# Performance work log

Hardware: AMD Instinct MI355X
Metric: run time of the kernel (lower is better)

Reference implementation:

```python
import jax, jax.numpy as jnp
import numpy as np

B, N, D = 8, 256, 256
LN_EPS = 1e-5


def setup_inputs() -> dict:
    key = jax.random.key(0)
    ks = jax.random.split(key, 8)
    s1 = 1.0 / np.sqrt(2 * D)  # torch Linear init scale ~ U(-1/sqrt(fan_in), ...); use normal*scale
    s2 = 1.0 / np.sqrt(D)
    return {
        "patch_features": jax.random.normal(ks[0], (B, N, D), dtype=jnp.float32),
        # relation_transform: Linear(2D, D) -> ReLU -> Linear(D, 1)
        "W1": jax.random.normal(ks[1], (2 * D, D), dtype=jnp.float32) * s1,
        "b1": jax.random.normal(ks[2], (D,), dtype=jnp.float32) * s1,
        "W2": jax.random.normal(ks[3], (D, 1), dtype=jnp.float32) * s2,
        "b2": jax.random.normal(ks[4], (1,), dtype=jnp.float32) * s2,
        # context_projection: Linear(D, D) + LayerNorm(D)
        "Wp": jax.random.normal(ks[5], (D, D), dtype=jnp.float32) * s2,
        "bp": jax.random.normal(ks[6], (D,), dtype=jnp.float32) * s2,
        "ln_gamma": jnp.ones((D,), dtype=jnp.float32),
        "ln_beta": jnp.zeros((D,), dtype=jnp.float32),
    }


def reference(patch_features, W1, b1, W2, b2, Wp, bp, ln_gamma, ln_beta):
    x = patch_features  # [B, N, D]
    d = x.shape[-1]
    # cat([x_i, x_j]) @ W1 == x_i @ W1[:D] + x_j @ W1[D:]
    hi = jnp.einsum("bnd,de->bne", x, W1[:d])   # [B, N, D]
    hj = jnp.einsum("bmd,de->bme", x, W1[d:])   # [B, N, D]
    h = jax.nn.relu(hi[:, :, None, :] + hj[:, None, :, :] + b1)  # [B, N, N, D]
    scores = jnp.einsum("bnmd,do->bnm", h, W2) + b2[0]            # [B, N, N]
    # diagonal entries stay exactly 0 (original never fills i == j)
    eye = jnp.eye(scores.shape[1], dtype=bool)
    scores = jnp.where(eye[None, :, :], 0.0, scores)
    weights = jax.nn.softmax(scores, axis=2)                      # [B, N, N]
    ctx = jnp.einsum("bnm,bmd->bnd", weights, x)                  # [B, N, D]
    proj = jnp.einsum("bnd,de->bne", ctx, Wp) + bp
    mu = jnp.mean(proj, axis=-1, keepdims=True)
    var = jnp.mean(jnp.square(proj - mu), axis=-1, keepdims=True)
    ln = (proj - mu) * jax.lax.rsqrt(var + LN_EPS) * ln_gamma + ln_beta
    return x + ln
```

## Files before the change

### kernel.cpp

```cpp
#include <hip/hip_runtime.h>

#define LN_EPS 1e-5f

__device__ __forceinline__ float wred_max(float v) {
#pragma unroll
    for (int off = 32; off; off >>= 1) v = fmaxf(v, __shfl_xor(v, off, 64));
    return v;
}
__device__ __forceinline__ float wred_sum(float v) {
#pragma unroll
    for (int off = 32; off; off >>= 1) v += __shfl_xor(v, off, 64);
    return v;
}


#define GL(Q, KB) { const float* _p = Wb + (size_t)((KB) * 8) * 256;            \
    _Pragma("unroll") for (int _j = 0; _j < 8; _j++)                            \
        Q[_j] = *(const float2*)(_p + (size_t)_j * 256); }

#define GC(Q, KB) { const int _k = (KB) * 8;                                    \
    _Pragma("unroll") for (int _r = 0; _r < 4; _r++) {                          \
        float4 _xa = *(const float4*)&xs[_r][_k];                               \
        float4 _xb = *(const float4*)&xs[_r][_k + 4];                           \
        acc[_r][0] = fmaf(_xa.x, Q[0].x, acc[_r][0]);                           \
        acc[_r][1] = fmaf(_xa.x, Q[0].y, acc[_r][1]);                           \
        acc[_r][0] = fmaf(_xa.y, Q[1].x, acc[_r][0]);                           \
        acc[_r][1] = fmaf(_xa.y, Q[1].y, acc[_r][1]);                           \
        acc[_r][0] = fmaf(_xa.z, Q[2].x, acc[_r][0]);                           \
        acc[_r][1] = fmaf(_xa.z, Q[2].y, acc[_r][1]);                           \
        acc[_r][0] = fmaf(_xa.w, Q[3].x, acc[_r][0]);                           \
        acc[_r][1] = fmaf(_xa.w, Q[3].y, acc[_r][1]);                           \
        acc[_r][0] = fmaf(_xb.x, Q[4].x, acc[_r][0]);                           \
        acc[_r][1] = fmaf(_xb.x, Q[4].y, acc[_r][1]);                           \
        acc[_r][0] = fmaf(_xb.y, Q[5].x, acc[_r][0]);                           \
        acc[_r][1] = fmaf(_xb.y, Q[5].y, acc[_r][1]);                           \
        acc[_r][0] = fmaf(_xb.z, Q[6].x, acc[_r][0]);                           \
        acc[_r][1] = fmaf(_xb.z, Q[6].y, acc[_r][1]);                           \
        acc[_r][0] = fmaf(_xb.w, Q[7].x, acc[_r][0]);                           \
        acc[_r][1] = fmaf(_xb.w, Q[7].y, acc[_r][1]); } }

__global__ __launch_bounds__(256) void k_gemm_hij(
    const float* __restrict__ x,
    const float* __restrict__ W1,
    const float* __restrict__ b1,
    float* __restrict__ hi_ws,
    float* __restrict__ hjT)
{
    __shared__ __align__(16) float xs[4][256];
    const int t = threadIdx.x;
    const int lane = t & 63, w = t >> 6;
    const int b = blockIdx.x & 7;
    const int i = blockIdx.x >> 3;
    const int row0 = b * 256 + i * 4;

    ((float4*)xs)[t] = ((const float4*)(x + (size_t)row0 * 256))[t];
    __syncthreads();

    const int half = w >> 1;
    const int e0 = ((w & 1) << 7) + 2 * lane;
    const float* Wb = W1 + (size_t)half * 65536 + e0;

    float acc[4][2];
#pragma unroll
    for (int r = 0; r < 4; r++) { acc[r][0] = 0.f; acc[r][1] = 0.f; }

    float2 qa[8], qb[8];
    GL(qa, 0);
    for (int kb = 0; kb + 2 < 32; kb += 2) {
        GL(qb, kb + 1);
        GC(qa, kb);
        GL(qa, kb + 2);
        GC(qb, kb + 1);
    }
    GL(qb, 31);
    GC(qa, 30);
    GC(qb, 31);

    if (half == 0) {
        float2 bb = *(const float2*)(b1 + e0);
#pragma unroll
        for (int r = 0; r < 4; r++)
            *(float2*)&hi_ws[(size_t)(row0 + r) * 256 + e0] =
                make_float2(acc[r][0] + bb.x, acc[r][1] + bb.y);
    } else {
        const int m0 = i * 4;
        *(float4*)&hjT[(size_t)b * 65536 + (size_t)e0 * 256 + m0] =
            make_float4(acc[0][0], acc[1][0], acc[2][0], acc[3][0]);
        *(float4*)&hjT[(size_t)b * 65536 + (size_t)(e0 + 1) * 256 + m0] =
            make_float4(acc[0][1], acc[1][1], acc[2][1], acc[3][1]);
    }
}


#define P1L(H, G) { const float* _p = hjp + (size_t)((G) * 4) * 256;            \
    _Pragma("unroll") for (int _j = 0; _j < 4; _j++)                            \
        H[_j] = *(const float4*)(_p + (size_t)_j * 256); }

#define P1C(H, G) { const int _db = w * 64 + (G) * 4;                           \
    float4 _wq = *(const float4*)&w2_s[_db];                                    \
    _Pragma("unroll") for (int _n = 0; _n < 4; _n++) {                          \
        float4 _h4 = *(const float4*)&hi_s[_n][_db];                            \
        sp[_n][0] = fmaf(fmaxf(_h4.x + H[0].x, 0.f), _wq.x, sp[_n][0]);         \
        sp[_n][0] = fmaf(fmaxf(_h4.y + H[1].x, 0.f), _wq.y, sp[_n][0]);         \
        sp[_n][0] = fmaf(fmaxf(_h4.z + H[2].x, 0.f), _wq.z, sp[_n][0]);         \
        sp[_n][0] = fmaf(fmaxf(_h4.w + H[3].x, 0.f), _wq.w, sp[_n][0]);         \
        sp[_n][1] = fmaf(fmaxf(_h4.x + H[0].y, 0.f), _wq.x, sp[_n][1]);         \
        sp[_n][1] = fmaf(fmaxf(_h4.y + H[1].y, 0.f), _wq.y, sp[_n][1]);         \
        sp[_n][1] = fmaf(fmaxf(_h4.z + H[2].y, 0.f), _wq.z, sp[_n][1]);         \
        sp[_n][1] = fmaf(fmaxf(_h4.w + H[3].y, 0.f), _wq.w, sp[_n][1]);         \
        sp[_n][2] = fmaf(fmaxf(_h4.x + H[0].z, 0.f), _wq.x, sp[_n][2]);         \
        sp[_n][2] = fmaf(fmaxf(_h4.y + H[1].z, 0.f), _wq.y, sp[_n][2]);         \
        sp[_n][2] = fmaf(fmaxf(_h4.z + H[2].z, 0.f), _wq.z, sp[_n][2]);         \
        sp[_n][2] = fmaf(fmaxf(_h4.w + H[3].z, 0.f), _wq.w, sp[_n][2]);         \
        sp[_n][3] = fmaf(fmaxf(_h4.x + H[0].w, 0.f), _wq.x, sp[_n][3]);         \
        sp[_n][3] = fmaf(fmaxf(_h4.y + H[1].w, 0.f), _wq.y, sp[_n][3]);         \
        sp[_n][3] = fmaf(fmaxf(_h4.z + H[2].w, 0.f), _wq.z, sp[_n][3]);         \
        sp[_n][3] = fmaf(fmaxf(_h4.w + H[3].w, 0.f), _wq.w, sp[_n][3]); } }

#define DLOAD(X, PTR, G) { const float* _p = (PTR) + (size_t)((G) * 8) * 256;   \
    _Pragma("unroll") for (int _j = 0; _j < 8; _j++)                            \
        X[_j] = *(const float4*)(_p + (size_t)_j * 256); }

#define DCOMP(ACCV, WS, X, G) { const int _rb = w * 64 + (G) * 8;               \
    _Pragma("unroll") for (int _n = 0; _n < 4; _n++) {                          \
        float4 _wa = *(const float4*)&WS[_n][_rb];                              \
        float4 _wb = *(const float4*)&WS[_n][_rb + 4];                          \
        ACCV[_n][0] = fmaf(_wa.x, X[0].x, ACCV[_n][0]);                         \
        ACCV[_n][0] = fmaf(_wa.y, X[1].x, ACCV[_n][0]);                         \
        ACCV[_n][0] = fmaf(_wa.z, X[2].x, ACCV[_n][0]);                         \
        ACCV[_n][0] = fmaf(_wa.w, X[3].x, ACCV[_n][0]);                         \
        ACCV[_n][0] = fmaf(_wb.x, X[4].x, ACCV[_n][0]);                         \
        ACCV[_n][0] = fmaf(_wb.y, X[5].x, ACCV[_n][0]);                         \
        ACCV[_n][0] = fmaf(_wb.z, X[6].x, ACCV[_n][0]);                         \
        ACCV[_n][0] = fmaf(_wb.w, X[7].x, ACCV[_n][0]);                         \
        ACCV[_n][1] = fmaf(_wa.x, X[0].y, ACCV[_n][1]);                         \
        ACCV[_n][1] = fmaf(_wa.y, X[1].y, ACCV[_n][1]);                         \
        ACCV[_n][1] = fmaf(_wa.z, X[2].y, ACCV[_n][1]);                         \
        ACCV[_n][1] = fmaf(_wa.w, X[3].y, ACCV[_n][1]);                         \
        ACCV[_n][1] = fmaf(_wb.x, X[4].y, ACCV[_n][1]);                         \
        ACCV[_n][1] = fmaf(_wb.y, X[5].y, ACCV[_n][1]);                         \
        ACCV[_n][1] = fmaf(_wb.z, X[6].y, ACCV[_n][1]);                         \
        ACCV[_n][1] = fmaf(_wb.w, X[7].y, ACCV[_n][1]);                         \
        ACCV[_n][2] = fmaf(_wa.x, X[0].z, ACCV[_n][2]);                         \
        ACCV[_n][2] = fmaf(_wa.y, X[1].z, ACCV[_n][2]);                         \
        ACCV[_n][2] = fmaf(_wa.z, X[2].z, ACCV[_n][2]);                         \
        ACCV[_n][2] = fmaf(_wa.w, X[3].z, ACCV[_n][2]);                         \
        ACCV[_n][2] = fmaf(_wb.x, X[4].z, ACCV[_n][2]);                         \
        ACCV[_n][2] = fmaf(_wb.y, X[5].z, ACCV[_n][2]);                         \
        ACCV[_n][2] = fmaf(_wb.z, X[6].z, ACCV[_n][2]);                         \
        ACCV[_n][2] = fmaf(_wb.w, X[7].z, ACCV[_n][2]);                         \
        ACCV[_n][3] = fmaf(_wa.x, X[0].w, ACCV[_n][3]);                         \
        ACCV[_n][3] = fmaf(_wa.y, X[1].w, ACCV[_n][3]);                         \
        ACCV[_n][3] = fmaf(_wa.z, X[2].w, ACCV[_n][3]);                         \
        ACCV[_n][3] = fmaf(_wa.w, X[3].w, ACCV[_n][3]);                         \
        ACCV[_n][3] = fmaf(_wb.x, X[4].w, ACCV[_n][3]);                         \
        ACCV[_n][3] = fmaf(_wb.y, X[5].w, ACCV[_n][3]);                         \
        ACCV[_n][3] = fmaf(_wb.z, X[6].w, ACCV[_n][3]);                         \
        ACCV[_n][3] = fmaf(_wb.w, X[7].w, ACCV[_n][3]); } }

__global__ __launch_bounds__(256) void k_fused(
    const float* __restrict__ x,
    const float* __restrict__ hi_ws,
    const float* __restrict__ hjT,
    const float* __restrict__ W2, const float* __restrict__ b2,
    const float* __restrict__ Wp, const float* __restrict__ bp,
    const float* __restrict__ gma, const float* __restrict__ bta,
    float* __restrict__ out)
{
    const int t = threadIdx.x;
    const int lane = t & 63, w = t >> 6;
    const int b = blockIdx.x & 7;
    const int n0 = (blockIdx.x >> 3) * 4;
    const int bn0 = b * 256 + n0;

    __shared__ __align__(16) float hi_s[4][256];
    __shared__ __align__(16) float w2_s[256];
    __shared__ __align__(16) float wt_s[4][256];
    __shared__ __align__(16) float ctx_s[4][256];
    __shared__ __align__(16) float sred[4][4][256];
    __shared__ float part[8][4];

#pragma unroll
    for (int i = 0; i < 4; i++) hi_s[i][t] = hi_ws[(size_t)(bn0 + i) * 256 + t];
    w2_s[t] = W2[t];
    __syncthreads();

    {
        const float* hjp = hjT + (size_t)b * 65536 + (size_t)(w * 64) * 256 + 4 * lane;
        float sp[4][4];
#pragma unroll
        for (int n = 0; n < 4; n++)
#pragma unroll
            for (int j = 0; j < 4; j++) sp[n][j] = 0.f;

        float4 ha[4], hb[4];
        P1L(ha, 0);
        for (int g = 0; g + 2 < 16; g += 2) {
            P1L(hb, g + 1);
            P1C(ha, g);
            P1L(ha, g + 2);
            P1C(hb, g + 1);
        }
        P1L(hb, 15);
        P1C(ha, 14);
        P1C(hb, 15);

#pragma unroll
        for (int n = 0; n < 4; n++)
            *(float4*)&sred[w][n][4 * lane] =
                make_float4(sp[n][0], sp[n][1], sp[n][2], sp[n][3]);
    }
    __syncthreads();

    float b2v = b2[0];
    float s[4];
#pragma unroll
    for (int i = 0; i < 4; i++) {
        s[i] = ((sred[0][i][t] + sred[1][i][t]) +
                (sred[2][i][t] + sred[3][i][t])) + b2v;
        if (t == n0 + i) s[i] = 0.f;
    }
#pragma unroll
    for (int i = 0; i < 4; i++) {
        float m = wred_max(s[i]);
        if (lane == 0) part[i][w] = m;
    }
    __syncthreads();
    float ev[4];
#pragma unroll
    for (int i = 0; i < 4; i++) {
        float mx = fmaxf(fmaxf(part[i][0], part[i][1]),
                         fmaxf(part[i][2], part[i][3]));
        ev[i] = __expf(s[i] - mx);
        float sm = wred_sum(ev[i]);
        if (lane == 0) part[4 + i][w] = sm;
    }
    __syncthreads();
#pragma unroll
    for (int i = 0; i < 4; i++) {
        float tot = (part[4 + i][0] + part[4 + i][1]) +
                    (part[4 + i][2] + part[4 + i][3]);
        wt_s[i][t] = ev[i] / tot;
    }
    __syncthreads();

    {
        const float* xpp = x + (size_t)b * 65536 + (size_t)(w * 64) * 256 + 4 * lane;
        float cp[4][4];
#pragma unroll
        for (int n = 0; n < 4; n++)
#pragma unroll
            for (int j = 0; j < 4; j++) cp[n][j] = 0.f;

        float4 xa[8], xb[8];
        DLOAD(xa, xpp, 0);
        for (int g = 0; g + 2 < 8; g += 2) {
            DLOAD(xb, xpp, g + 1);
            DCOMP(cp, wt_s, xa, g);
            DLOAD(xa, xpp, g + 2);
            DCOMP(cp, wt_s, xb, g + 1);
        }
        DLOAD(xb, xpp, 7);
        DCOMP(cp, wt_s, xa, 6);
        DCOMP(cp, wt_s, xb, 7);

#pragma unroll
        for (int n = 0; n < 4; n++)
            *(float4*)&sred[w][n][4 * lane] =
                make_float4(cp[n][0], cp[n][1], cp[n][2], cp[n][3]);
    }
    __syncthreads();
#pragma unroll
    for (int i = 0; i < 4; i++)
        ctx_s[i][t] = (sred[0][i][t] + sred[1][i][t]) +
                      (sred[2][i][t] + sred[3][i][t]);
    __syncthreads();

    {
        const float* wpp = Wp + (size_t)(w * 64) * 256 + 4 * lane;
        float pq[4][4];
#pragma unroll
        for (int n = 0; n < 4; n++)
#pragma unroll
            for (int j = 0; j < 4; j++) pq[n][j] = 0.f;

        float4 qa4[8], qb4[8];
        DLOAD(qa4, wpp, 0);
        for (int g = 0; g + 2 < 8; g += 2) {
            DLOAD(qb4, wpp, g + 1);
            DCOMP(pq, ctx_s, qa4, g);
            DLOAD(qa4, wpp, g + 2);
            DCOMP(pq, ctx_s, qb4, g + 1);
        }
        DLOAD(qb4, wpp, 7);
        DCOMP(pq, ctx_s, qa4, 6);
        DCOMP(pq, ctx_s, qb4, 7);

#pragma unroll
        for (int n = 0; n < 4; n++)
            *(float4*)&sred[w][n][4 * lane] =
                make_float4(pq[n][0], pq[n][1], pq[n][2], pq[n][3]);
    }
    __syncthreads();

    float bpv = bp[t];
    float p[4];
#pragma unroll
    for (int i = 0; i < 4; i++)
        p[i] = ((sred[0][i][t] + sred[1][i][t]) +
                (sred[2][i][t] + sred[3][i][t])) + bpv;

#pragma unroll
    for (int i = 0; i < 4; i++) {
        float su = wred_sum(p[i]);
        float sq = wred_sum(p[i] * p[i]);
        if (lane == 0) { part[i][w] = su; part[4 + i][w] = sq; }
    }
    __syncthreads();
    float gv = gma[t], bv = bta[t];
#pragma unroll
    for (int i = 0; i < 4; i++) {
        float su = (part[i][0] + part[i][1]) + (part[i][2] + part[i][3]);
        float sq = (part[4 + i][0] + part[4 + i][1]) +
                   (part[4 + i][2] + part[4 + i][3]);
        float mu = su * (1.f / 256.f);
        float var = sq * (1.f / 256.f) - mu * mu;
        float ln = (p[i] - mu) * rsqrtf(var + LN_EPS) * gv + bv;
        out[(size_t)(bn0 + i) * 256 + t] = x[(size_t)(bn0 + i) * 256 + t] + ln;
    }
}

extern "C" void kernel_launch(void* const* d_in, const int* in_sizes, int n_in,
                              void* d_out, int out_size, void* d_ws, size_t ws_size,
                              hipStream_t stream) {
    const float* x   = (const float*)d_in[0];
    const float* W1  = (const float*)d_in[1];
    const float* b1  = (const float*)d_in[2];
    const float* W2  = (const float*)d_in[3];
    const float* b2  = (const float*)d_in[4];
    const float* Wp  = (const float*)d_in[5];
    const float* bp  = (const float*)d_in[6];
    const float* gma = (const float*)d_in[7];
    const float* bta = (const float*)d_in[8];
    float* out = (float*)d_out;

    float* hi_ws = (float*)d_ws;
    float* hjT   = hi_ws + (size_t)2048 * 256;

    k_gemm_hij<<<512, 256, 0, stream>>>(x, W1, b1, hi_ws, hjT);
    k_fused<<<512, 256, 0, stream>>>(x, hi_ws, hjT, W2, b2, Wp, bp,
                                     gma, bta, out);
}
```

Baseline: 107.5 us.

## Retile hij GEMM and widen fused kernel to 8 rows per 512-thread block

The first GEMM kernel is re-tiled so each wave computes 8 rows by 64 output columns. X rows are read directly from global memory (uniform per wave) instead of through shared memory, and W1 is loaded as scalar columns. The fused scoring/softmax/projection kernel now handles 8 query rows per block with 512 threads, so each thread reuses its loaded hjT, x and Wp values across twice as many rows, halving redundant global reads. The cost is more shared memory, extra barriers for the two-pass reductions, higher register pressure, and half as many blocks.

```diff
diff --git a/kernel.cpp b/kernel.cpp
--- a/kernel.cpp
+++ b/kernel.cpp
@@ -14,30 +14,13 @@
 }
 
 
-#define GL(Q, KB) { const float* _p = Wb + (size_t)((KB) * 8) * 256;            \
-    _Pragma("unroll") for (int _j = 0; _j < 8; _j++)                            \
-        Q[_j] = *(const float2*)(_p + (size_t)_j * 256); }
-
-#define GC(Q, KB) { const int _k = (KB) * 8;                                    \
-    _Pragma("unroll") for (int _r = 0; _r < 4; _r++) {                          \
-        float4 _xa = *(const float4*)&xs[_r][_k];                               \
-        float4 _xb = *(const float4*)&xs[_r][_k + 4];                           \
-        acc[_r][0] = fmaf(_xa.x, Q[0].x, acc[_r][0]);                           \
-        acc[_r][1] = fmaf(_xa.x, Q[0].y, acc[_r][1]);                           \
-        acc[_r][0] = fmaf(_xa.y, Q[1].x, acc[_r][0]);                           \
-        acc[_r][1] = fmaf(_xa.y, Q[1].y, acc[_r][1]);                           \
-        acc[_r][0] = fmaf(_xa.z, Q[2].x, acc[_r][0]);                           \
-        acc[_r][1] = fmaf(_xa.z, Q[2].y, acc[_r][1]);                           \
-        acc[_r][0] = fmaf(_xa.w, Q[3].x, acc[_r][0]);                           \
-        acc[_r][1] = fmaf(_xa.w, Q[3].y, acc[_r][1]);                           \
-        acc[_r][0] = fmaf(_xb.x, Q[4].x, acc[_r][0]);                           \
-        acc[_r][1] = fmaf(_xb.x, Q[4].y, acc[_r][1]);                           \
-        acc[_r][0] = fmaf(_xb.y, Q[5].x, acc[_r][0]);                           \
-        acc[_r][1] = fmaf(_xb.y, Q[5].y, acc[_r][1]);                           \
-        acc[_r][0] = fmaf(_xb.z, Q[6].x, acc[_r][0]);                           \
-        acc[_r][1] = fmaf(_xb.z, Q[6].y, acc[_r][1]);                           \
-        acc[_r][0] = fmaf(_xb.w, Q[7].x, acc[_r][0]);                           \
-        acc[_r][1] = fmaf(_xb.w, Q[7].y, acc[_r][1]); } }
+#define WL(Q, KB) { _Pragma("unroll") for (int _j = 0; _j < 8; _j++)            \
+        Q[_j] = Wc[(size_t)((KB) * 8 + _j) * 256]; }
+
+#define XC(Q, KB) { _Pragma("unroll") for (int _j = 0; _j < 8; _j++) {          \
+        const float _wj = Q[_j];                                                \
+        _Pragma("unroll") for (int _r = 0; _r < 8; _r++)                        \
+            acc[_r] = fmaf(xw[_r * 256 + (KB) * 8 + _j], _wj, acc[_r]); } }
 
 __global__ __launch_bounds__(256) void k_gemm_hij(
     const float* __restrict__ x,
@@ -46,48 +29,45 @@
     float* __restrict__ hi_ws,
     float* __restrict__ hjT)
 {
-    __shared__ __align__(16) float xs[4][256];
     const int t = threadIdx.x;
-    const int lane = t & 63, w = t >> 6;
-    const int b = blockIdx.x & 7;
-    const int i = blockIdx.x >> 3;
-    const int row0 = b * 256 + i * 4;
-
-    ((float4*)xs)[t] = ((const float4*)(x + (size_t)row0 * 256))[t];
-    __syncthreads();
-
-    const int half = w >> 1;
-    const int e0 = ((w & 1) << 7) + 2 * lane;
-    const float* Wb = W1 + (size_t)half * 65536 + e0;
-
-    float acc[4][2];
-#pragma unroll
-    for (int r = 0; r < 4; r++) { acc[r][0] = 0.f; acc[r][1] = 0.f; }
-
-    float2 qa[8], qb[8];
-    GL(qa, 0);
+    const int lane = t & 63;
+    const int w = __builtin_amdgcn_readfirstlane(t >> 6);
+    const int b  = blockIdx.x & 7;
+    const int rg = (blockIdx.x >> 3) & 7;
+    const int cg = blockIdx.x >> 6;
+
+    const int m0 = rg * 32 + w * 8;
+    const int row0 = b * 256 + m0;
+    const int e = cg * 64 + lane;
+
+    const float* xw = x + (size_t)row0 * 256;
+    const float* Wc = W1 + e + (e >= 256 ? 65280 : 0);
+
+    float acc[8];
+#pragma unroll
+    for (int r = 0; r < 8; r++) acc[r] = 0.f;
+
+    float qa[8], qb[8];
+    WL(qa, 0);
     for (int kb = 0; kb + 2 < 32; kb += 2) {
-        GL(qb, kb + 1);
-        GC(qa, kb);
-        GL(qa, kb + 2);
-        GC(qb, kb + 1);
-    }
-    GL(qb, 31);
-    GC(qa, 30);
-    GC(qb, 31);
-
-    if (half == 0) {
-        float2 bb = *(const float2*)(b1 + e0);
-#pragma unroll
-        for (int r = 0; r < 4; r++)
-            *(float2*)&hi_ws[(size_t)(row0 + r) * 256 + e0] =
-                make_float2(acc[r][0] + bb.x, acc[r][1] + bb.y);
+        WL(qb, kb + 1);
+        XC(qa, kb);
+        WL(qa, kb + 2);
+        XC(qb, kb + 1);
+    }
+    WL(qb, 31);
+    XC(qa, 30);
+    XC(qb, 31);
+
+    if (e < 256) {
+        const float bb = b1[e];
+#pragma unroll
+        for (int r = 0; r < 8; r++)
+            hi_ws[(size_t)(row0 + r) * 256 + e] = acc[r] + bb;
     } else {
-        const int m0 = i * 4;
-        *(float4*)&hjT[(size_t)b * 65536 + (size_t)e0 * 256 + m0] =
-            make_float4(acc[0][0], acc[1][0], acc[2][0], acc[3][0]);
-        *(float4*)&hjT[(size_t)b * 65536 + (size_t)(e0 + 1) * 256 + m0] =
-            make_float4(acc[0][1], acc[1][1], acc[2][1], acc[3][1]);
+        float* dst = hjT + (size_t)b * 65536 + (size_t)(e - 256) * 256 + m0;
+        *(float4*)dst       = make_float4(acc[0], acc[1], acc[2], acc[3]);
+        *(float4*)(dst + 4) = make_float4(acc[4], acc[5], acc[6], acc[7]);
     }
 }
 
@@ -96,9 +76,9 @@
     _Pragma("unroll") for (int _j = 0; _j < 4; _j++)                            \
         H[_j] = *(const float4*)(_p + (size_t)_j * 256); }
 
-#define P1C(H, G) { const int _db = w * 64 + (G) * 4;                           \
+#define P1C(H, G) { const int _db = w * 32 + (G) * 4;                           \
     float4 _wq = *(const float4*)&w2_s[_db];                                    \
-    _Pragma("unroll") for (int _n = 0; _n < 4; _n++) {                          \
+    _Pragma("unroll") for (int _n = 0; _n < 8; _n++) {                          \
         float4 _h4 = *(const float4*)&hi_s[_n][_db];                            \
         sp[_n][0] = fmaf(fmaxf(_h4.x + H[0].x, 0.f), _wq.x, sp[_n][0]);         \
         sp[_n][0] = fmaf(fmaxf(_h4.y + H[1].x, 0.f), _wq.y, sp[_n][0]);         \
@@ -121,8 +101,8 @@
     _Pragma("unroll") for (int _j = 0; _j < 8; _j++)                            \
         X[_j] = *(const float4*)(_p + (size_t)_j * 256); }
 
-#define DCOMP(ACCV, WS, X, G) { const int _rb = w * 64 + (G) * 8;               \
-    _Pragma("unroll") for (int _n = 0; _n < 4; _n++) {                          \
+#define DCOMP(ACCV, WS, X, G) { const int _rb = w * 32 + (G) * 8;               \
+    _Pragma("unroll") for (int _n = 0; _n < 8; _n++) {                          \
         float4 _wa = *(const float4*)&WS[_n][_rb];                              \
         float4 _wb = *(const float4*)&WS[_n][_rb + 4];                          \
         ACCV[_n][0] = fmaf(_wa.x, X[0].x, ACCV[_n][0]);                         \
@@ -158,7 +138,7 @@
         ACCV[_n][3] = fmaf(_wb.z, X[6].w, ACCV[_n][3]);                         \
         ACCV[_n][3] = fmaf(_wb.w, X[7].w, ACCV[_n][3]); } }
 
-__global__ __launch_bounds__(256) void k_fused(
+__global__ __launch_bounds__(512) void k_fused(
     const float* __restrict__ x,
     const float* __restrict__ hi_ws,
     const float* __restrict__ hjT,
@@ -170,163 +150,209 @@
     const int t = threadIdx.x;
     const int lane = t & 63, w = t >> 6;
     const int b = blockIdx.x & 7;
-    const int n0 = (blockIdx.x >> 3) * 4;
+    const int n0 = (blockIdx.x >> 3) * 8;
     const int bn0 = b * 256 + n0;
 
-    __shared__ __align__(16) float hi_s[4][256];
+    __shared__ __align__(16) float hi_s[8][256];
     __shared__ __align__(16) float w2_s[256];
-    __shared__ __align__(16) float wt_s[4][256];
-    __shared__ __align__(16) float ctx_s[4][256];
-    __shared__ __align__(16) float sred[4][4][256];
-    __shared__ float part[8][4];
-
-#pragma unroll
-    for (int i = 0; i < 4; i++) hi_s[i][t] = hi_ws[(size_t)(bn0 + i) * 256 + t];
-    w2_s[t] = W2[t];
+    __shared__ __align__(16) float wt_s[8][256];
+    __shared__ __align__(16) float ctx_s[8][256];
+    __shared__ __align__(16) float sred[8][4][256];
+    __shared__ float part_a[8][4], part_b[8][4];
+
+    ((float4*)hi_s)[t] = ((const float4*)(hi_ws + (size_t)bn0 * 256))[t];
+    if (t < 64) ((float4*)w2_s)[t] = ((const float4*)W2)[t];
     __syncthreads();
 
-    {
-        const float* hjp = hjT + (size_t)b * 65536 + (size_t)(w * 64) * 256 + 4 * lane;
-        float sp[4][4];
-#pragma unroll
-        for (int n = 0; n < 4; n++)
+    const int m = t & 255;
+    const int h = t >> 8;
+    const int wg = w & 3;
+
+    float sA[2], sB[2];
+    {
+        const float* hjp = hjT + (size_t)b * 65536 + (size_t)(w * 32) * 256 + 4 * lane;
+        float sp[8][4];
+#pragma unroll
+        for (int n = 0; n < 8; n++)
 #pragma unroll
             for (int j = 0; j < 4; j++) sp[n][j] = 0.f;
 
         float4 ha[4], hb[4];
         P1L(ha, 0);
-        for (int g = 0; g + 2 < 16; g += 2) {
-            P1L(hb, g + 1);
-            P1C(ha, g);
-            P1L(ha, g + 2);
-            P1C(hb, g + 1);
-        }
-        P1L(hb, 15);
-        P1C(ha, 14);
-        P1C(hb, 15);
-
+        P1L(hb, 1); P1C(ha, 0);
+        P1L(ha, 2); P1C(hb, 1);
+        P1L(hb, 3); P1C(ha, 2);
+        P1L(ha, 4); P1C(hb, 3);
+        P1L(hb, 5); P1C(ha, 4);
+        P1L(ha, 6); P1C(hb, 5);
+        P1L(hb, 7); P1C(ha, 6);
+        P1C(hb, 7);
+
+        const float b2v = b2[0];
 #pragma unroll
         for (int n = 0; n < 4; n++)
             *(float4*)&sred[w][n][4 * lane] =
                 make_float4(sp[n][0], sp[n][1], sp[n][2], sp[n][3]);
+        __syncthreads();
+#pragma unroll
+        for (int c = 0; c < 2; c++) {
+            const int n = 2 * h + c;
+            float v = ((sred[0][n][m] + sred[1][n][m]) + (sred[2][n][m] + sred[3][n][m])) +
+                      ((sred[4][n][m] + sred[5][n][m]) + (sred[6][n][m] + sred[7][n][m]));
+            v += b2v;
+            if (m == n0 + n) v = 0.f;
+            sA[c] = v;
+        }
+        __syncthreads();
+#pragma unroll
+        for (int n = 0; n < 4; n++)
+            *(float4*)&sred[w][n][4 * lane] =
+                make_float4(sp[4 + n][0], sp[4 + n][1], sp[4 + n][2], sp[4 + n][3]);
+        __syncthreads();
+#pragma unroll
+        for (int c = 0; c < 2; c++) {
+            const int nn = 2 * h + c;
+            float v = ((sred[0][nn][m] + sred[1][nn][m]) + (sred[2][nn][m] + sred[3][nn][m])) +
+                      ((sred[4][nn][m] + sred[5][nn][m]) + (sred[6][nn][m] + sred[7][nn][m]));
+            v += b2v;
+            if (m == n0 + 4 + nn) v = 0.f;
+            sB[c] = v;
+        }
+    }
+
+    {
+        const int ns[4] = {2 * h, 2 * h + 1, 4 + 2 * h, 4 + 2 * h + 1};
+        float s4[4] = {sA[0], sA[1], sB[0], sB[1]};
+        float ev4[4];
+#pragma unroll
+        for (int c = 0; c < 4; c++) {
+            const float mxw = wred_max(s4[c]);
+            if (lane == 0) part_a[ns[c]][wg] = mxw;
+        }
+        __syncthreads();
+#pragma unroll
+        for (int c = 0; c < 4; c++) {
+            const int n = ns[c];
+            const float mx = fmaxf(fmaxf(part_a[n][0], part_a[n][1]),
+                                   fmaxf(part_a[n][2], part_a[n][3]));
+            ev4[c] = __expf(s4[c] - mx);
+            const float sm = wred_sum(ev4[c]);
+            if (lane == 0) part_b[n][wg] = sm;
+        }
+        __syncthreads();
+#pragma unroll
+        for (int c = 0; c < 4; c++) {
+            const int n = ns[c];
+            const float tot = (part_b[n][0] + part_b[n][1]) + (part_b[n][2] + part_b[n][3]);
+            wt_s[n][m] = ev4[c] / tot;
+        }
     }
     __syncthreads();
 
-    float b2v = b2[0];
-    float s[4];
-#pragma unroll
-    for (int i = 0; i < 4; i++) {
-        s[i] = ((sred[0][i][t] + sred[1][i][t]) +
-                (sred[2][i][t] + sred[3][i][t])) + b2v;
-        if (t == n0 + i) s[i] = 0.f;
-    }
-#pragma unroll
-    for (int i = 0; i < 4; i++) {
-        float m = wred_max(s[i]);
-        if (lane == 0) part[i][w] = m;
-    }
-    __syncthreads();
-    float ev[4];
-#pragma unroll
-    for (int i = 0; i < 4; i++) {
-        float mx = fmaxf(fmaxf(part[i][0], part[i][1]),
-                         fmaxf(part[i][2], part[i][3]));
-        ev[i] = __expf(s[i] - mx);
-        float sm = wred_sum(ev[i]);
-        if (lane == 0) part[4 + i][w] = sm;
-    }
-    __syncthreads();
-#pragma unroll
-    for (int i = 0; i < 4; i++) {
-        float tot = (part[4 + i][0] + part[4 + i][1]) +
-                    (part[4 + i][2] + part[4 + i][3]);
-        wt_s[i][t] = ev[i] / tot;
-    }
-    __syncthreads();
-
-    {
-        const float* xpp = x + (size_t)b * 65536 + (size_t)(w * 64) * 256 + 4 * lane;
-        float cp[4][4];
-#pragma unroll
-        for (int n = 0; n < 4; n++)
+    {
+        const float* xpp = x + (size_t)b * 65536 + (size_t)(w * 32) * 256 + 4 * lane;
+        float cp[8][4];
+#pragma unroll
+        for (int n = 0; n < 8; n++)
 #pragma unroll
             for (int j = 0; j < 4; j++) cp[n][j] = 0.f;
 
         float4 xa[8], xb[8];
         DLOAD(xa, xpp, 0);
-        for (int g = 0; g + 2 < 8; g += 2) {
-            DLOAD(xb, xpp, g + 1);
-            DCOMP(cp, wt_s, xa, g);
-            DLOAD(xa, xpp, g + 2);
-            DCOMP(cp, wt_s, xb, g + 1);
-        }
-        DLOAD(xb, xpp, 7);
-        DCOMP(cp, wt_s, xa, 6);
-        DCOMP(cp, wt_s, xb, 7);
+        DLOAD(xb, xpp, 1); DCOMP(cp, wt_s, xa, 0);
+        DLOAD(xa, xpp, 2); DCOMP(cp, wt_s, xb, 1);
+        DLOAD(xb, xpp, 3); DCOMP(cp, wt_s, xa, 2);
+        DCOMP(cp, wt_s, xb, 3);
 
 #pragma unroll
         for (int n = 0; n < 4; n++)
             *(float4*)&sred[w][n][4 * lane] =
                 make_float4(cp[n][0], cp[n][1], cp[n][2], cp[n][3]);
+        __syncthreads();
+#pragma unroll
+        for (int c = 0; c < 2; c++) {
+            const int n = 2 * h + c;
+            ctx_s[n][m] = ((sred[0][n][m] + sred[1][n][m]) + (sred[2][n][m] + sred[3][n][m])) +
+                          ((sred[4][n][m] + sred[5][n][m]) + (sred[6][n][m] + sred[7][n][m]));
+        }
+        __syncthreads();
+#pragma unroll
+        for (int n = 0; n < 4; n++)
+            *(float4*)&sred[w][n][4 * lane] =
+                make_float4(cp[4 + n][0], cp[4 + n][1], cp[4 + n][2], cp[4 + n][3]);
+        __syncthreads();
+#pragma unroll
+        for (int c = 0; c < 2; c++) {
+            const int nn = 2 * h + c;
+            ctx_s[4 + nn][m] = ((sred[0][nn][m] + sred[1][nn][m]) + (sred[2][nn][m] + sred[3][nn][m])) +
+                               ((sred[4][nn][m] + sred[5][nn][m]) + (sred[6][nn][m] + sred[7][nn][m]));
+        }
     }
     __syncthreads();
-#pragma unroll
-    for (int i = 0; i < 4; i++)
-        ctx_s[i][t] = (sred[0][i][t] + sred[1][i][t]) +
-                      (sred[2][i][t] + sred[3][i][t]);
-    __syncthreads();
-
-    {
-        const float* wpp = Wp + (size_t)(w * 64) * 256 + 4 * lane;
-        float pq[4][4];
-#pragma unroll
-        for (int n = 0; n < 4; n++)
+
+    float p4[4];
+    {
+        const float* wpp = Wp + (size_t)(w * 32) * 256 + 4 * lane;
+        float pq[8][4];
+#pragma unroll
+        for (int n = 0; n < 8; n++)
 #pragma unroll
             for (int j = 0; j < 4; j++) pq[n][j] = 0.f;
 
         float4 qa4[8], qb4[8];
         DLOAD(qa4, wpp, 0);
-        for (int g = 0; g + 2 < 8; g += 2) {
-            DLOAD(qb4, wpp, g + 1);
-            DCOMP(pq, ctx_s, qa4, g);
-            DLOAD(qa4, wpp, g + 2);
-            DCOMP(pq, ctx_s, qb4, g + 1);
-        }
-        DLOAD(qb4, wpp, 7);
-        DCOMP(pq, ctx_s, qa4, 6);
-        DCOMP(pq, ctx_s, qb4, 7);
-
+        DLOAD(qb4, wpp, 1); DCOMP(pq, ctx_s, qa4, 0);
+        DLOAD(qa4, wpp, 2); DCOMP(pq, ctx_s, qb4, 1);
+        DLOAD(qb4, wpp, 3); DCOMP(pq, ctx_s, qa4, 2);
+        DCOMP(pq, ctx_s, qb4, 3);
+
+        const float bpv = bp[m];
 #pragma unroll
         for (int n = 0; n < 4; n++)
             *(float4*)&sred[w][n][4 * lane] =
                 make_float4(pq[n][0], pq[n][1], pq[n][2], pq[n][3]);
-    }
-    __syncthreads();
-
-    float bpv = bp[t];
-    float p[4];
-#pragma unroll
-    for (int i = 0; i < 4; i++)
-        p[i] = ((sred[0][i][t] + sred[1][i][t]) +
-                (sred[2][i][t] + sred[3][i][t])) + bpv;
-
-#pragma unroll
-    for (int i = 0; i < 4; i++) {
-        float su = wred_sum(p[i]);
-        float sq = wred_sum(p[i] * p[i]);
-        if (lane == 0) { part[i][w] = su; part[4 + i][w] = sq; }
-    }
-    __syncthreads();
-    float gv = gma[t], bv = bta[t];
-#pragma unroll
-    for (int i = 0; i < 4; i++) {
-        float su = (part[i][0] + part[i][1]) + (part[i][2] + part[i][3]);
-        float sq = (part[4 + i][0] + part[4 + i][1]) +
-                   (part[4 + i][2] + part[4 + i][3]);
-        float mu = su * (1.f / 256.f);
-        float var = sq * (1.f / 256.f) - mu * mu;
-        float ln = (p[i] - mu) * rsqrtf(var + LN_EPS) * gv + bv;
-        out[(size_t)(bn0 + i) * 256 + t] = x[(size_t)(bn0 + i) * 256 + t] + ln;
+        __syncthreads();
+#pragma unroll
+        for (int c = 0; c < 2; c++) {
+            const int n = 2 * h + c;
+            p4[c] = ((sred[0][n][m] + sred[1][n][m]) + (sred[2][n][m] + sred[3][n][m])) +
+                    ((sred[4][n][m] + sred[5][n][m]) + (sred[6][n][m] + sred[7][n][m])) + bpv;
+        }
+        __syncthreads();
+#pragma unroll
+        for (int n = 0; n < 4; n++)
+            *(float4*)&sred[w][n][4 * lane] =
+                make_float4(pq[4 + n][0], pq[4 + n][1], pq[4 + n][2], pq[4 + n][3]);
+        __syncthreads();
+#pragma unroll
+        for (int c = 0; c < 2; c++) {
+            const int nn = 2 * h + c;
+            p4[2 + c] = ((sred[0][nn][m] + sred[1][nn][m]) + (sred[2][nn][m] + sred[3][nn][m])) +
+                        ((sred[4][nn][m] + sred[5][nn][m]) + (sred[6][nn][m] + sred[7][nn][m])) + bpv;
+        }
+    }
+
+    {
+        const int ns[4] = {2 * h, 2 * h + 1, 4 + 2 * h, 4 + 2 * h + 1};
+#pragma unroll
+        for (int c = 0; c < 4; c++) {
+            const float su = wred_sum(p4[c]);
+            const float sq = wred_sum(p4[c] * p4[c]);
+            if (lane == 0) { part_a[ns[c]][wg] = su; part_b[ns[c]][wg] = sq; }
+        }
+        __syncthreads();
+        const float gv = gma[m], bv = bta[m];
+#pragma unroll
+        for (int c = 0; c < 4; c++) {
+            const int n = ns[c];
+            const float su = (part_a[n][0] + part_a[n][1]) + (part_a[n][2] + part_a[n][3]);
+            const float sq = (part_b[n][0] + part_b[n][1]) + (part_b[n][2] + part_b[n][3]);
+            const float mu = su * (1.f / 256.f);
+            const float var = sq * (1.f / 256.f) - mu * mu;
+            const float ln = (p4[c] - mu) * rsqrtf(var + LN_EPS) * gv + bv;
+            const size_t off = (size_t)(bn0 + n) * 256 + m;
+            out[off] = x[off] + ln;
+        }
     }
 }
 
@@ -348,6 +374,6 @@
     float* hjT   = hi_ws + (size_t)2048 * 256;
 
     k_gemm_hij<<<512, 256, 0, stream>>>(x, W1, b1, hi_ws, hjT);
-    k_fused<<<512, 256, 0, stream>>>(x, hi_ws, hjT, W2, b2, Wp, bp,
+    k_fused<<<256, 512, 0, stream>>>(x, hi_ws, hjT, W2, b2, Wp, bp,
                                      gma, bta, out);
 }
```

New measurement: 195.8 us. 1.82x slower.

## Process eight query rows per block in fused kernel to halve hjT reloads

Applied to the files above, without the earlier changes.

The fused kernel now handles 8 rows of n per block instead of 4, so grid size drops from 512 to 256. Each hjT, x and Wp element loaded from global memory is reused across twice as many rows. The goal is to halve global/L2 traffic in the pairwise-score phase, which dominates. In exchange the block uses more registers and shared memory (launch_bounds(256,1)), and with 256 blocks on a 256-CU part occupancy and latency hiding may fall.

```diff
diff --git a/kernel.cpp b/kernel.cpp
--- a/kernel.cpp
+++ b/kernel.cpp
@@ -98,7 +98,7 @@
 
 #define P1C(H, G) { const int _db = w * 64 + (G) * 4;                           \
     float4 _wq = *(const float4*)&w2_s[_db];                                    \
-    _Pragma("unroll") for (int _n = 0; _n < 4; _n++) {                          \
+    _Pragma("unroll") for (int _n = 0; _n < 8; _n++) {                          \
         float4 _h4 = *(const float4*)&hi_s[_n][_db];                            \
         sp[_n][0] = fmaf(fmaxf(_h4.x + H[0].x, 0.f), _wq.x, sp[_n][0]);         \
         sp[_n][0] = fmaf(fmaxf(_h4.y + H[1].x, 0.f), _wq.y, sp[_n][0]);         \
@@ -117,48 +117,31 @@
         sp[_n][3] = fmaf(fmaxf(_h4.z + H[2].w, 0.f), _wq.z, sp[_n][3]);         \
         sp[_n][3] = fmaf(fmaxf(_h4.w + H[3].w, 0.f), _wq.w, sp[_n][3]); } }
 
-#define DLOAD(X, PTR, G) { const float* _p = (PTR) + (size_t)((G) * 8) * 256;   \
-    _Pragma("unroll") for (int _j = 0; _j < 8; _j++)                            \
+#define P2L(X, PTR, G) { const float* _p = (PTR) + (size_t)((G) * 4) * 256;     \
+    _Pragma("unroll") for (int _j = 0; _j < 4; _j++)                            \
         X[_j] = *(const float4*)(_p + (size_t)_j * 256); }
 
-#define DCOMP(ACCV, WS, X, G) { const int _rb = w * 64 + (G) * 8;               \
-    _Pragma("unroll") for (int _n = 0; _n < 4; _n++) {                          \
+#define P2C(ACCV, WS, X, G) { const int _rb = w * 64 + (G) * 4;                 \
+    _Pragma("unroll") for (int _n = 0; _n < 8; _n++) {                          \
         float4 _wa = *(const float4*)&WS[_n][_rb];                              \
-        float4 _wb = *(const float4*)&WS[_n][_rb + 4];                          \
         ACCV[_n][0] = fmaf(_wa.x, X[0].x, ACCV[_n][0]);                         \
         ACCV[_n][0] = fmaf(_wa.y, X[1].x, ACCV[_n][0]);                         \
         ACCV[_n][0] = fmaf(_wa.z, X[2].x, ACCV[_n][0]);                         \
         ACCV[_n][0] = fmaf(_wa.w, X[3].x, ACCV[_n][0]);                         \
-        ACCV[_n][0] = fmaf(_wb.x, X[4].x, ACCV[_n][0]);                         \
-        ACCV[_n][0] = fmaf(_wb.y, X[5].x, ACCV[_n][0]);                         \
-        ACCV[_n][0] = fmaf(_wb.z, X[6].x, ACCV[_n][0]);                         \
-        ACCV[_n][0] = fmaf(_wb.w, X[7].x, ACCV[_n][0]);                         \
         ACCV[_n][1] = fmaf(_wa.x, X[0].y, ACCV[_n][1]);                         \
         ACCV[_n][1] = fmaf(_wa.y, X[1].y, ACCV[_n][1]);                         \
         ACCV[_n][1] = fmaf(_wa.z, X[2].y, ACCV[_n][1]);                         \
         ACCV[_n][1] = fmaf(_wa.w, X[3].y, ACCV[_n][1]);                         \
-        ACCV[_n][1] = fmaf(_wb.x, X[4].y, ACCV[_n][1]);                         \
-        ACCV[_n][1] = fmaf(_wb.y, X[5].y, ACCV[_n][1]);                         \
-        ACCV[_n][1] = fmaf(_wb.z, X[6].y, ACCV[_n][1]);                         \
-        ACCV[_n][1] = fmaf(_wb.w, X[7].y, ACCV[_n][1]);                         \
         ACCV[_n][2] = fmaf(_wa.x, X[0].z, ACCV[_n][2]);                         \
         ACCV[_n][2] = fmaf(_wa.y, X[1].z, ACCV[_n][2]);                         \
         ACCV[_n][2] = fmaf(_wa.z, X[2].z, ACCV[_n][2]);                         \
         ACCV[_n][2] = fmaf(_wa.w, X[3].z, ACCV[_n][2]);                         \
-        ACCV[_n][2] = fmaf(_wb.x, X[4].z, ACCV[_n][2]);                         \
-        ACCV[_n][2] = fmaf(_wb.y, X[5].z, ACCV[_n][2]);                         \
-        ACCV[_n][2] = fmaf(_wb.z, X[6].z, ACCV[_n][2]);                         \
-        ACCV[_n][2] = fmaf(_wb.w, X[7].z, ACCV[_n][2]);                         \
         ACCV[_n][3] = fmaf(_wa.x, X[0].w, ACCV[_n][3]);                         \
         ACCV[_n][3] = fmaf(_wa.y, X[1].w, ACCV[_n][3]);                         \
         ACCV[_n][3] = fmaf(_wa.z, X[2].w, ACCV[_n][3]);                         \
-        ACCV[_n][3] = fmaf(_wa.w, X[3].w, ACCV[_n][3]);                         \
-        ACCV[_n][3] = fmaf(_wb.x, X[4].w, ACCV[_n][3]);                         \
-        ACCV[_n][3] = fmaf(_wb.y, X[5].w, ACCV[_n][3]);                         \
-        ACCV[_n][3] = fmaf(_wb.z, X[6].w, ACCV[_n][3]);                         \
-        ACCV[_n][3] = fmaf(_wb.w, X[7].w, ACCV[_n][3]); } }
-
-__global__ __launch_bounds__(256) void k_fused(
+        ACCV[_n][3] = fmaf(_wa.w, X[3].w, ACCV[_n][3]); } }
+
+__global__ __launch_bounds__(256, 1) void k_fused(
     const float* __restrict__ x,
     const float* __restrict__ hi_ws,
     const float* __restrict__ hjT,
@@ -170,26 +153,29 @@
     const int t = threadIdx.x;
     const int lane = t & 63, w = t >> 6;
     const int b = blockIdx.x & 7;
-    const int n0 = (blockIdx.x >> 3) * 4;
+    const int n0 = (blockIdx.x >> 3) * 8;
     const int bn0 = b * 256 + n0;
 
-    __shared__ __align__(16) float hi_s[4][256];
+    __shared__ __align__(16) float hi_s[8][256];
     __shared__ __align__(16) float w2_s[256];
-    __shared__ __align__(16) float wt_s[4][256];
-    __shared__ __align__(16) float ctx_s[4][256];
-    __shared__ __align__(16) float sred[4][4][256];
-    __shared__ float part[8][4];
-
-#pragma unroll
-    for (int i = 0; i < 4; i++) hi_s[i][t] = hi_ws[(size_t)(bn0 + i) * 256 + t];
+    __shared__ __align__(16) float wt_s[8][256];
+    __shared__ __align__(16) float ctx_s[8][256];
+    __shared__ __align__(16) float sred[4][8][256];
+    __shared__ float part_a[8][4], part_b[8][4];
+
+    {
+        const float4* src = (const float4*)(hi_ws + (size_t)bn0 * 256);
+        ((float4*)hi_s)[t]       = src[t];
+        ((float4*)hi_s)[t + 256] = src[t + 256];
+    }
     w2_s[t] = W2[t];
     __syncthreads();
 
     {
         const float* hjp = hjT + (size_t)b * 65536 + (size_t)(w * 64) * 256 + 4 * lane;
-        float sp[4][4];
-#pragma unroll
-        for (int n = 0; n < 4; n++)
+        float sp[8][4];
+#pragma unroll
+        for (int n = 0; n < 8; n++)
 #pragma unroll
             for (int j = 0; j < 4; j++) sp[n][j] = 0.f;
 
@@ -206,127 +192,126 @@
         P1C(hb, 15);
 
 #pragma unroll
-        for (int n = 0; n < 4; n++)
+        for (int n = 0; n < 8; n++)
             *(float4*)&sred[w][n][4 * lane] =
                 make_float4(sp[n][0], sp[n][1], sp[n][2], sp[n][3]);
     }
     __syncthreads();
 
-    float b2v = b2[0];
-    float s[4];
-#pragma unroll
-    for (int i = 0; i < 4; i++) {
-        s[i] = ((sred[0][i][t] + sred[1][i][t]) +
-                (sred[2][i][t] + sred[3][i][t])) + b2v;
-        if (t == n0 + i) s[i] = 0.f;
-    }
-#pragma unroll
-    for (int i = 0; i < 4; i++) {
-        float m = wred_max(s[i]);
-        if (lane == 0) part[i][w] = m;
-    }
-    __syncthreads();
-    float ev[4];
-#pragma unroll
-    for (int i = 0; i < 4; i++) {
-        float mx = fmaxf(fmaxf(part[i][0], part[i][1]),
-                         fmaxf(part[i][2], part[i][3]));
-        ev[i] = __expf(s[i] - mx);
-        float sm = wred_sum(ev[i]);
-        if (lane == 0) part[4 + i][w] = sm;
-    }
-    __syncthreads();
-#pragma unroll
-    for (int i = 0; i < 4; i++) {
-        float tot = (part[4 + i][0] + part[4 + i][1]) +
-                    (part[4 + i][2] + part[4 + i][3]);
-        wt_s[i][t] = ev[i] / tot;
+    const float b2v = b2[0];
+    float s[8], ev[8];
+#pragma unroll
+    for (int n = 0; n < 8; n++) {
+        s[n] = ((sred[0][n][t] + sred[1][n][t]) +
+                (sred[2][n][t] + sred[3][n][t])) + b2v;
+        if (t == n0 + n) s[n] = 0.f;
+    }
+#pragma unroll
+    for (int n = 0; n < 8; n++) {
+        const float mxw = wred_max(s[n]);
+        if (lane == 0) part_a[n][w] = mxw;
+    }
+    __syncthreads();
+#pragma unroll
+    for (int n = 0; n < 8; n++) {
+        const float mx = fmaxf(fmaxf(part_a[n][0], part_a[n][1]),
+                               fmaxf(part_a[n][2], part_a[n][3]));
+        ev[n] = __expf(s[n] - mx);
+        const float sm = wred_sum(ev[n]);
+        if (lane == 0) part_b[n][w] = sm;
+    }
+    __syncthreads();
+#pragma unroll
+    for (int n = 0; n < 8; n++) {
+        const float tot = (part_b[n][0] + part_b[n][1]) +
+                          (part_b[n][2] + part_b[n][3]);
+        wt_s[n][t] = ev[n] / tot;
     }
     __syncthreads();
 
     {
         const float* xpp = x + (size_t)b * 65536 + (size_t)(w * 64) * 256 + 4 * lane;
-        float cp[4][4];
-#pragma unroll
-        for (int n = 0; n < 4; n++)
+        float cp[8][4];
+#pragma unroll
+        for (int n = 0; n < 8; n++)
 #pragma unroll
             for (int j = 0; j < 4; j++) cp[n][j] = 0.f;
 
-        float4 xa[8], xb[8];
-        DLOAD(xa, xpp, 0);
-        for (int g = 0; g + 2 < 8; g += 2) {
-            DLOAD(xb, xpp, g + 1);
-            DCOMP(cp, wt_s, xa, g);
-            DLOAD(xa, xpp, g + 2);
-            DCOMP(cp, wt_s, xb, g + 1);
+        float4 xa[4], xb[4];
+        P2L(xa, xpp, 0);
+        for (int g = 0; g + 2 < 16; g += 2) {
+            P2L(xb, xpp, g + 1);
+            P2C(cp, wt_s, xa, g);
+            P2L(xa, xpp, g + 2);
+            P2C(cp, wt_s, xb, g + 1);
         }
-        DLOAD(xb, xpp, 7);
-        DCOMP(cp, wt_s, xa, 6);
-        DCOMP(cp, wt_s, xb, 7);
-
-#pragma unroll
-        for (int n = 0; n < 4; n++)
+        P2L(xb, xpp, 15);
+        P2C(cp, wt_s, xa, 14);
+        P2C(cp, wt_s, xb, 15);
+
+#pragma unroll
+        for (int n = 0; n < 8; n++)
             *(float4*)&sred[w][n][4 * lane] =
                 make_float4(cp[n][0], cp[n][1], cp[n][2], cp[n][3]);
     }
     __syncthreads();
 #pragma unroll
-    for (int i = 0; i < 4; i++)
-        ctx_s[i][t] = (sred[0][i][t] + sred[1][i][t]) +
-                      (sred[2][i][t] + sred[3][i][t]);
+    for (int n = 0; n < 8; n++)
+        ctx_s[n][t] = (sred[0][n][t] + sred[1][n][t]) +
+                      (sred[2][n][t] + sred[3][n][t]);
     __syncthreads();
 
     {
         const float* wpp = Wp + (size_t)(w * 64) * 256 + 4 * lane;
-        float pq[4][4];
-#pragma unroll
-        for (int n = 0; n < 4; n++)
+        float pq[8][4];
+#pragma unroll
+        for (int n = 0; n < 8; n++)
 #pragma unroll
             for (int j = 0; j < 4; j++) pq[n][j] = 0.f;
 
-        float4 qa4[8], qb4[8];
-        DLOAD(qa4, wpp, 0);
-        for (int g = 0; g + 2 < 8; g += 2) {
-            DLOAD(qb4, wpp, g + 1);
-            DCOMP(pq, ctx_s, qa4, g);
-            DLOAD(qa4, wpp, g + 2);
-            DCOMP(pq, ctx_s, qb4, g + 1);
+        float4 qa4[4], qb4[4];
+        P2L(qa4, wpp, 0);
+        for (int g = 0; g + 2 < 16; g += 2) {
+            P2L(qb4, wpp, g + 1);
+            P2C(pq, ctx_s, qa4, g);
+            P2L(qa4, wpp, g + 2);
+            P2C(pq, ctx_s, qb4, g + 1);
         }
-        DLOAD(qb4, wpp, 7);
-        DCOMP(pq, ctx_s, qa4, 6);
-        DCOMP(pq, ctx_s, qb4, 7);
-
-#pragma unroll
-        for (int n = 0; n < 4; n++)
+        P2L(qb4, wpp, 15);
+        P2C(pq, ctx_s, qa4, 14);
+        P2C(pq, ctx_s, qb4, 15);
+
+#pragma unroll
+        for (int n = 0; n < 8; n++)
             *(float4*)&sred[w][n][4 * lane] =
                 make_float4(pq[n][0], pq[n][1], pq[n][2], pq[n][3]);
     }
     __syncthreads();
 
-    float bpv = bp[t];
-    float p[4];
-#pragma unroll
-    for (int i = 0; i < 4; i++)
-        p[i] = ((sred[0][i][t] + sred[1][i][t]) +
-                (sred[2][i][t] + sred[3][i][t])) + bpv;
-
-#pragma unroll
-    for (int i = 0; i < 4; i++) {
-        float su = wred_sum(p[i]);
-        float sq = wred_sum(p[i] * p[i]);
-        if (lane == 0) { part[i][w] = su; part[4 + i][w] = sq; }
-    }
-    __syncthreads();
-    float gv = gma[t], bv = bta[t];
-#pragma unroll
-    for (int i = 0; i < 4; i++) {
-        float su = (part[i][0] + part[i][1]) + (part[i][2] + part[i][3]);
-        float sq = (part[4 + i][0] + part[4 + i][1]) +
-                   (part[4 + i][2] + part[4 + i][3]);
-        float mu = su * (1.f / 256.f);
-        float var = sq * (1.f / 256.f) - mu * mu;
-        float ln = (p[i] - mu) * rsqrtf(var + LN_EPS) * gv + bv;
-        out[(size_t)(bn0 + i) * 256 + t] = x[(size_t)(bn0 + i) * 256 + t] + ln;
+    const float bpv = bp[t];
+    float p[8];
+#pragma unroll
+    for (int n = 0; n < 8; n++)
+        p[n] = ((sred[0][n][t] + sred[1][n][t]) +
+                (sred[2][n][t] + sred[3][n][t])) + bpv;
+
+#pragma unroll
+    for (int n = 0; n < 8; n++) {
+        const float su = wred_sum(p[n]);
+        const float sq = wred_sum(p[n] * p[n]);
+        if (lane == 0) { part_a[n][w] = su; part_b[n][w] = sq; }
+    }
+    __syncthreads();
+    const float gv = gma[t], bv = bta[t];
+#pragma unroll
+    for (int n = 0; n < 8; n++) {
+        const float su = (part_a[n][0] + part_a[n][1]) + (part_a[n][2] + part_a[n][3]);
+        const float sq = (part_b[n][0] + part_b[n][1]) + (part_b[n][2] + part_b[n][3]);
+        const float mu = su * (1.f / 256.f);
+        const float var = sq * (1.f / 256.f) - mu * mu;
+        const float ln = (p[n] - mu) * rsqrtf(var + LN_EPS) * gv + bv;
+        const size_t off = (size_t)(bn0 + n) * 256 + t;
+        out[off] = x[off] + ln;
     }
 }
 
@@ -348,6 +333,6 @@
     float* hjT   = hi_ws + (size_t)2048 * 256;
 
     k_gemm_hij<<<512, 256, 0, stream>>>(x, W1, b1, hi_ws, hjT);
-    k_fused<<<512, 256, 0, stream>>>(x, hi_ws, hjT, W2, b2, Wp, bp,
+    k_fused<<<256, 256, 0, stream>>>(x, hi_ws, hjT, W2, b2, Wp, bp,
                                      gma, bta, out);
 }
```

New measurement: 115.2 us. +7.2%, slower.
